# Kernel tuning notes

Measured on AMD Instinct MI355X. Metric: run time of the kernel, lower is better.

The kernel has to match this reference:

```python
import jax, jax.numpy as jnp
import numpy as np

B, E, DIM = 8, 2048, 512
KERNEL = 8
DECAY_CONSTANT = 1.0


def _forward(x, weight, bias, decay_value):
    # x: (B, E, S) with S == dim; weight: (K, S); bias: (S,); decay_value: (2, 1)
    K, dim = weight.shape
    Bb, Ee, S = x.shape
    i = jnp.arange(dim)[:, None]
    j = jnp.arange(dim)[None, :]
    # decayed upper-triangular weight: W[k, i, j] = weight[k, j] * dv^((j-i)/c) for j >= i
    dv = jnp.clip(decay_value[1, 0], 0.9, 1.0)
    d = dv ** ((j - i).astype(x.dtype) / DECAY_CONSTANT)  # (S, S)
    W = jnp.where(j >= i, weight[:, None, :] * d[None], jnp.zeros((), x.dtype))  # (K, S, S)
    p = K - 1
    padded = jnp.pad(x, ((0, 0), (p, p), (0, 0)))  # zero-pad sequence axis
    # shifted stack: stacked[b, k, e] = x[b, e + k - (K-1)] (zeros out of range) -> causal taps
    stacked = jnp.stack([padded[:, k:Ee + k] for k in range(K)], axis=1)  # (B, K, E, S)
    out = jnp.einsum('bkei,kij->bej', stacked, W) + bias
    return out


def setup_inputs() -> dict:
    key = jax.random.key(0)
    k1, k2 = jax.random.split(key)
    x = jax.random.normal(k1, (B, E, DIM), dtype=jnp.float32)
    weight = jax.random.normal(k2, (KERNEL, DIM), dtype=jnp.float32)
    bias = jnp.zeros((DIM,), dtype=jnp.float32)
    decay_value = jnp.ones((2, 1), dtype=jnp.float32)
    return {"x": x, "weight": weight, "bias": bias, "decay_value": decay_value}


def reference(x, weight, bias, decay_value):
    return _forward(x, weight, bias, decay_value)
```

## Files before the change

### kernel.cpp

```cpp
#include <hip/hip_runtime.h>


#define B_     8
#define E_     2048
#define DIM_   512
#define K_     8
#define TILE_E 32
#define NROWS  (TILE_E + K_ - 1)
#define LSTR   516
#define NF4    (NROWS * (DIM_ / 4))

__global__ __launch_bounds__(256) void krl_t(
    const float* __restrict__ x,
    const float* __restrict__ weight,
    const float* __restrict__ bias,
    const float* __restrict__ decay,
    float* __restrict__ out)
{
    __shared__ float yls[NROWS * LSTR];

    const int t  = threadIdx.x;
    const int b  = blockIdx.y;
    const int e0 = blockIdx.x * TILE_E;

    const int ebase = e0 - (K_ - 1);
    for (int i = t; i < NF4; i += 256) {
        const int r  = i >> 7;
        const int f4 = i & 127;
        const int eg = ebase + r;
        float4 v = make_float4(0.f, 0.f, 0.f, 0.f);
        if (eg >= 0)
            v = *(const float4*)(x + ((size_t)b * E_ + eg) * DIM_ + f4 * 4);
        *(float4*)(&yls[r * LSTR + f4 * 4]) = v;
    }

    float dv = decay[1];
    dv = fminf(fmaxf(dv, 0.9f), 1.0f);
    const float d1 = dv, d2 = dv * dv, d3 = d2 * dv, d4 = d2 * d2;
    float d128 = d4;
    d128 *= d128; d128 *= d128; d128 *= d128; d128 *= d128; d128 *= d128;
    const float d256 = d128 * d128;

    __syncthreads();

    const int lane = t & 63, wave = t >> 6;
    const int r16 = lane & 15, seg = lane >> 4;
    const int row = wave * 16 + r16;
    if (row < NROWS) {
        float* sp = &yls[row * LSTR + seg * 128];

        float E = 0.f;
        #pragma unroll 8
        for (int q = 0; q < 32; ++q) {
            const float4 v = *(const float4*)(sp + 4 * q);
            const float p = fmaf(d3, v.x, fmaf(d2, v.y, fmaf(d1, v.z, v.w)));
            E = fmaf(d4, E, p);
        }

        float S = E;
        float u1 = __shfl_up(S, 16, 64); if (seg >= 1) S = fmaf(d128, u1, S);
        float u2 = __shfl_up(S, 32, 64); if (seg >= 2) S = fmaf(d256, u2, S);
        float C = __shfl_up(S, 16, 64);  if (seg == 0) C = 0.f;

        float prev = C;
        #pragma unroll 8
        for (int q = 0; q < 32; ++q) {
            const float4 v = *(const float4*)(sp + 4 * q);
            const float p01   = fmaf(d1, v.x, v.y);
            const float p012  = fmaf(d1, p01, v.z);
            const float p0123 = fmaf(d1, p012, v.w);
            float4 yv;
            yv.x = fmaf(d1, prev, v.x);
            yv.y = fmaf(d2, prev, p01);
            yv.z = fmaf(d3, prev, p012);
            yv.w = fmaf(d4, prev, p0123);
            prev = yv.w;
            *(float4*)(sp + 4 * q) = yv;
        }
    }

    const int j  = t & 127, h = t >> 7;
    const int jf = j * 4;
    float4 w[K_];
    #pragma unroll
    for (int k = 0; k < K_; ++k) w[k] = *(const float4*)(weight + k * DIM_ + jf);
    const float4 bi = *(const float4*)(bias + jf);

    __syncthreads();

    const int te0 = h * 16;
    float4 win[K_];
    #pragma unroll
    for (int k = 0; k < 7; ++k)
        win[k] = *(const float4*)(&yls[(te0 + k) * LSTR + jf]);

    #pragma unroll
    for (int i = 0; i < 16; ++i) {
        const int te = te0 + i;
        win[7] = *(const float4*)(&yls[(te + 7) * LSTR + jf]);
        float4 acc = bi;
        #pragma unroll
        for (int k = 0; k < K_; ++k) {
            acc.x = fmaf(w[k].x, win[k].x, acc.x);
            acc.y = fmaf(w[k].y, win[k].y, acc.y);
            acc.z = fmaf(w[k].z, win[k].z, acc.z);
            acc.w = fmaf(w[k].w, win[k].w, acc.w);
        }
        *(float4*)(out + ((size_t)b * E_ + e0 + te) * DIM_ + jf) = acc;
        #pragma unroll
        for (int k = 0; k < 7; ++k) win[k] = win[k + 1];
    }
}

extern "C" void kernel_launch(void* const* d_in, const int* in_sizes, int n_in,
                              void* d_out, int out_size, void* d_ws, size_t ws_size,
                              hipStream_t stream) {
    const float* x      = (const float*)d_in[0];
    const float* weight = (const float*)d_in[1];
    const float* bias   = (const float*)d_in[2];
    const float* decay  = (const float*)d_in[3];
    float* out = (float*)d_out;

    dim3 grid(E_ / TILE_E, B_);
    dim3 block(256);
    krl_t<<<grid, block, 0, stream>>>(x, weight, bias, decay, out);
}
```

Baseline: 91.25 us.

## Process 64-row strips with async LDS prefetch overlapping scan and conv

Each block now handles a 64-row strip in two 32-row halves, with 512 threads. The second half is prefetched straight into LDS with global_load_lds while the first half is scanned and convolved. This halves the redundant halo rows per output and hides global-load latency behind compute. In exchange it uses much more LDS per block (about 146KB), which limits residency to one block per CU, and it relies on hand-written waitcnt/barrier asm whose vmcnt count must match the issued loads.

```diff
diff --git a/kernel.cpp b/kernel.cpp
--- a/kernel.cpp
+++ b/kernel.cpp
@@ -1,38 +1,112 @@
 #include <hip/hip_runtime.h>
 
 
-#define B_     8
-#define E_     2048
-#define DIM_   512
-#define K_     8
-#define TILE_E 32
-#define NROWS  (TILE_E + K_ - 1)
-#define LSTR   516
-#define NF4    (NROWS * (DIM_ / 4))
+#define B_    8
+#define E_    2048
+#define DIM_  512
+#define K_    8
+#define TE    32
+#define STRIP 64
+#define HALO  (K_ - 1)
+#define NRA   (TE + HALO)
+#define NRB   TE
+#define LSTR  516
+#define NF4A  (NRA * 128)
+#define NF4B  (NRB * 128)
 
-__global__ __launch_bounds__(256) void krl_t(
+typedef __attribute__((address_space(1))) const float gfloat_t;
+typedef __attribute__((address_space(3))) float       sfloat_t;
+
+__device__ __forceinline__ void gld16(float* lds, const float* g)
+{
+    __builtin_amdgcn_global_load_lds((gfloat_t*)g, (sfloat_t*)lds, 16, 0, 0);
+}
+
+__device__ __forceinline__ void scan_rows(float* __restrict__ yls, int rowbase,
+    int nrows, int t, float d1, float d2, float d3, float d4,
+    float d128, float d256)
+{
+    const int lane = t & 63, wave = t >> 6;
+    const int r16 = lane & 15, seg = lane >> 4;
+    const int rw  = wave * 16 + r16;
+    if (rw >= nrows) return;
+    float* sp = &yls[(rowbase + rw) * LSTR + seg * 128];
+
+    float E = 0.f;
+    #pragma unroll 8
+    for (int q = 0; q < 32; ++q) {
+        const float4 v = *(const float4*)(sp + 4 * q);
+        const float p = fmaf(d3, v.x, fmaf(d2, v.y, fmaf(d1, v.z, v.w)));
+        E = fmaf(d4, E, p);
+    }
+    float S = E;
+    float u1 = __shfl_up(S, 16, 64); if (seg >= 1) S = fmaf(d128, u1, S);
+    float u2 = __shfl_up(S, 32, 64); if (seg >= 2) S = fmaf(d256, u2, S);
+    float C  = __shfl_up(S, 16, 64); if (seg == 0) C = 0.f;
+    float prev = C;
+    #pragma unroll 8
+    for (int q = 0; q < 32; ++q) {
+        const float4 v = *(const float4*)(sp + 4 * q);
+        const float p01   = fmaf(d1, v.x, v.y);
+        const float p012  = fmaf(d1, p01, v.z);
+        const float p0123 = fmaf(d1, p012, v.w);
+        float4 yv;
+        yv.x = fmaf(d1, prev, v.x);
+        yv.y = fmaf(d2, prev, p01);
+        yv.z = fmaf(d3, prev, p012);
+        yv.w = fmaf(d4, prev, p0123);
+        prev = yv.w;
+        *(float4*)(sp + 4 * q) = yv;
+    }
+}
+
+__device__ __forceinline__ void conv8(const float* __restrict__ yls,
+    float* __restrict__ out, int b, int e0, int o0, int jf,
+    const float4 (&w)[K_], float4 bi)
+{
+    float4 win[K_];
+    #pragma unroll
+    for (int k = 0; k < 7; ++k)
+        win[k] = *(const float4*)(&yls[(o0 + k) * LSTR + jf]);
+    #pragma unroll
+    for (int i = 0; i < 8; ++i) {
+        const int o = o0 + i;
+        win[7] = *(const float4*)(&yls[(o + 7) * LSTR + jf]);
+        float4 acc = bi;
+        #pragma unroll
+        for (int k = 0; k < K_; ++k) {
+            acc.x = fmaf(w[k].x, win[k].x, acc.x);
+            acc.y = fmaf(w[k].y, win[k].y, acc.y);
+            acc.z = fmaf(w[k].z, win[k].z, acc.z);
+            acc.w = fmaf(w[k].w, win[k].w, acc.w);
+        }
+        *(float4*)(out + ((size_t)b * E_ + e0 + o) * DIM_ + jf) = acc;
+        #pragma unroll
+        for (int k = 0; k < 7; ++k) win[k] = win[k + 1];
+    }
+}
+
+__global__ __launch_bounds__(512) void krl_p(
     const float* __restrict__ x,
     const float* __restrict__ weight,
     const float* __restrict__ bias,
     const float* __restrict__ decay,
     float* __restrict__ out)
 {
-    __shared__ float yls[NROWS * LSTR];
+    __shared__ float yls[(NRA + NRB) * LSTR];
 
     const int t  = threadIdx.x;
     const int b  = blockIdx.y;
-    const int e0 = blockIdx.x * TILE_E;
+    const int e0 = blockIdx.x * STRIP;
+    const int ebase = e0 - HALO;
+    const float* xb = x + (size_t)b * E_ * DIM_;
 
-    const int ebase = e0 - (K_ - 1);
-    for (int i = t; i < NF4; i += 256) {
-        const int r  = i >> 7;
-        const int f4 = i & 127;
-        const int eg = ebase + r;
-        float4 v = make_float4(0.f, 0.f, 0.f, 0.f);
-        if (eg >= 0)
-            v = *(const float4*)(x + ((size_t)b * E_ + eg) * DIM_ + f4 * 4);
-        *(float4*)(&yls[r * LSTR + f4 * 4]) = v;
-    }
+    const int j = t & 127, h = t >> 7;
+    const int jf = j * 4;
+    float4 w[K_];
+    #pragma unroll
+    for (int k = 0; k < K_; ++k) w[k] = *(const float4*)(weight + k * DIM_ + jf);
+    const float4 bi = *(const float4*)(bias + jf);
 
     float dv = decay[1];
     dv = fminf(fmaxf(dv, 0.9f), 1.0f);
@@ -41,75 +115,34 @@
     d128 *= d128; d128 *= d128; d128 *= d128; d128 *= d128; d128 *= d128;
     const float d256 = d128 * d128;
 
+    for (int i = t; i < NF4A; i += 512) {
+        const int r = i >> 7, f4 = i & 127;
+        const int eg = ebase + r;
+        float* lp = &yls[r * LSTR + f4 * 4];
+        if (eg >= 0) gld16(lp, xb + (size_t)eg * DIM_ + f4 * 4);
+        else         *(float4*)lp = make_float4(0.f, 0.f, 0.f, 0.f);
+    }
     __syncthreads();
 
-    const int lane = t & 63, wave = t >> 6;
-    const int r16 = lane & 15, seg = lane >> 4;
-    const int row = wave * 16 + r16;
-    if (row < NROWS) {
-        float* sp = &yls[row * LSTR + seg * 128];
-
-        float E = 0.f;
-        #pragma unroll 8
-        for (int q = 0; q < 32; ++q) {
-            const float4 v = *(const float4*)(sp + 4 * q);
-            const float p = fmaf(d3, v.x, fmaf(d2, v.y, fmaf(d1, v.z, v.w)));
-            E = fmaf(d4, E, p);
-        }
-
-        float S = E;
-        float u1 = __shfl_up(S, 16, 64); if (seg >= 1) S = fmaf(d128, u1, S);
-        float u2 = __shfl_up(S, 32, 64); if (seg >= 2) S = fmaf(d256, u2, S);
-        float C = __shfl_up(S, 16, 64);  if (seg == 0) C = 0.f;
-
-        float prev = C;
-        #pragma unroll 8
-        for (int q = 0; q < 32; ++q) {
-            const float4 v = *(const float4*)(sp + 4 * q);
-            const float p01   = fmaf(d1, v.x, v.y);
-            const float p012  = fmaf(d1, p01, v.z);
-            const float p0123 = fmaf(d1, p012, v.w);
-            float4 yv;
-            yv.x = fmaf(d1, prev, v.x);
-            yv.y = fmaf(d2, prev, p01);
-            yv.z = fmaf(d3, prev, p012);
-            yv.w = fmaf(d4, prev, p0123);
-            prev = yv.w;
-            *(float4*)(sp + 4 * q) = yv;
-        }
+    for (int i = t; i < NF4B; i += 512) {
+        const int r = i >> 7, f4 = i & 127;
+        gld16(&yls[(NRA + r) * LSTR + f4 * 4],
+              xb + (size_t)(e0 + TE + r) * DIM_ + f4 * 4);
     }
 
-    const int j  = t & 127, h = t >> 7;
-    const int jf = j * 4;
-    float4 w[K_];
-    #pragma unroll
-    for (int k = 0; k < K_; ++k) w[k] = *(const float4*)(weight + k * DIM_ + jf);
-    const float4 bi = *(const float4*)(bias + jf);
+    scan_rows(yls, 0, NRA, t, d1, d2, d3, d4, d128, d256);
 
-    __syncthreads();
+    asm volatile("s_waitcnt lgkmcnt(0)\n\ts_barrier" ::: "memory");
 
-    const int te0 = h * 16;
-    float4 win[K_];
-    #pragma unroll
-    for (int k = 0; k < 7; ++k)
-        win[k] = *(const float4*)(&yls[(te0 + k) * LSTR + jf]);
+    conv8(yls, out, b, e0, h * 8, jf, w, bi);
 
-    #pragma unroll
-    for (int i = 0; i < 16; ++i) {
-        const int te = te0 + i;
-        win[7] = *(const float4*)(&yls[(te + 7) * LSTR + jf]);
-        float4 acc = bi;
-        #pragma unroll
-        for (int k = 0; k < K_; ++k) {
-            acc.x = fmaf(w[k].x, win[k].x, acc.x);
-            acc.y = fmaf(w[k].y, win[k].y, acc.y);
-            acc.z = fmaf(w[k].z, win[k].z, acc.z);
-            acc.w = fmaf(w[k].w, win[k].w, acc.w);
-        }
-        *(float4*)(out + ((size_t)b * E_ + e0 + te) * DIM_ + jf) = acc;
-        #pragma unroll
-        for (int k = 0; k < 7; ++k) win[k] = win[k + 1];
-    }
+    asm volatile("s_waitcnt vmcnt(8)\n\ts_barrier" ::: "memory");
+
+    scan_rows(yls, NRA, NRB, t, d1, d2, d3, d4, d128, d256);
+
+    asm volatile("s_waitcnt lgkmcnt(0)\n\ts_barrier" ::: "memory");
+
+    conv8(yls, out, b, e0, 32 + h * 8, jf, w, bi);
 }
 
 extern "C" void kernel_launch(void* const* d_in, const int* in_sizes, int n_in,
@@ -121,7 +154,7 @@
     const float* decay  = (const float*)d_in[3];
     float* out = (float*)d_out;
 
-    dim3 grid(E_ / TILE_E, B_);
-    dim3 block(256);
-    krl_t<<<grid, block, 0, stream>>>(x, weight, bias, decay, out);
+    dim3 grid(E_ / STRIP, B_);
+    dim3 block(512);
+    krl_p<<<grid, block, 0, stream>>>(x, weight, bias, decay, out);
 }
```

New measurement: 90.96 us. No clear change (-0.3%).
